# Performance work log

Hardware: AMD Instinct MI355X
Metric: run time of the kernel (lower is better)

## Reference

```python
import jax, jax.numpy as jnp
import numpy as np

B, T, D = 16, 4096, 768
S_MAX = 128  # max sentence (segment) count per sample


def setup_inputs() -> dict:
    key = jax.random.key(0)
    ks = jax.random.split(key, 8)
    hidden = jax.random.normal(ks[0], (B, T, D), dtype=jnp.float32)
    # sorted per-token segment ids == cumulative torch.split span structure
    seg_ids = jnp.sort(jax.random.randint(ks[1], (B, T), 0, S_MAX, dtype=jnp.int32), axis=-1)
    s1, s2, s3 = 1.0 / np.sqrt(D), 1.0 / np.sqrt(384), 1.0 / np.sqrt(128)
    W1 = jax.random.normal(ks[2], (D, 384), dtype=jnp.float32) * s1
    b1 = jnp.zeros((384,), dtype=jnp.float32)
    W2 = jax.random.normal(ks[3], (384, 128), dtype=jnp.float32) * s2
    b2 = jnp.zeros((128,), dtype=jnp.float32)
    W3 = jax.random.normal(ks[4], (128, 2), dtype=jnp.float32) * s3
    b3 = jnp.zeros((2,), dtype=jnp.float32)
    return {"hidden": hidden, "seg_ids": seg_ids, "W1": W1, "b1": b1,
            "W2": W2, "b2": b2, "W3": W3, "b3": b3}


def reference(hidden, seg_ids, W1, b1, W2, b2, W3, b3):
    # split_tensor: per-sample segment-sum over token spans, padded to S_MAX.
    # Segments with no tokens come out zero, matching F.pad of the torch code.
    sent_em = jax.vmap(
        lambda h, s: jax.ops.segment_sum(h, s, num_segments=S_MAX)
    )(hidden, seg_ids)  # [B, S_MAX, D]
    # sent_pred MLP head
    x = jax.nn.relu(jnp.einsum('bsd,df->bsf', sent_em, W1) + b1)
    x = jax.nn.relu(jnp.einsum('bsf,fg->bsg', x, W2) + b2)
    pred = jnp.einsum('bsg,gc->bsc', x, W3) + b3  # [B, S_MAX, 2]
    return pred.reshape(B * S_MAX, -1)
```

## Files before the change

### kernel.cpp

```cpp
#include <hip/hip_runtime.h>

#define BATCH 16
#define TOK   4096
#define DIM   768
#define SMAX  128
#define BM    8

__device__ __forceinline__ int lower_bound_i(const int* __restrict__ a, int n, int v) {
    int lo = 0, hi = n;
    while (lo < hi) {
        int m = (lo + hi) >> 1;
        if (a[m] < v) lo = m + 1; else hi = m;
    }
    return lo;
}

__device__ __forceinline__ float f4get(const float4& v, int k) {
    switch (k) {
        case 0: return v.x;
        case 1: return v.y;
        case 2: return v.z;
        default: return v.w;
    }
}

__device__ __forceinline__ void f2acc(float2& a, const float2& v) {
    a.x += v.x; a.y += v.y;
}

__global__ __launch_bounds__(192)
void bounds_kernel(const int* __restrict__ seg, int* __restrict__ bounds) {
    const int b = blockIdx.x;
    const int s = threadIdx.x;
    if (s <= SMAX)
        bounds[b * (SMAX + 1) + s] = lower_bound_i(seg + b * TOK, TOK, s);
}

__global__ __launch_bounds__(1024)
void fused_kernel(const float* __restrict__ hidden,
                  const int* __restrict__ bounds,
                  const float* __restrict__ W1, const float* __restrict__ b1,
                  const float* __restrict__ W2, const float* __restrict__ b2,
                  const float* __restrict__ W3, const float* __restrict__ b3,
                  float* __restrict__ out) {
    __shared__ __align__(16) float A [BM * DIM];
    __shared__ __align__(16) float X1[BM * 384];
    __shared__ __align__(16) float X2[BM * 128];
    __shared__ __align__(16) float P [8 * BM * 384];

    const int tid  = threadIdx.x;
    const int row0 = blockIdx.x * BM;
    const int b    = row0 / SMAX;
    const int s0   = row0 % SMAX;

    {
        const int grp  = tid >> 7;
        const int lane = tid & 127;

        const int lo = bounds[b * (SMAX + 1) + s0 + grp];
        const int hi = bounds[b * (SMAX + 1) + s0 + grp + 1];

        const float2* __restrict__ hp =
            reinterpret_cast<const float2*>(hidden + (size_t)b * TOK * DIM) + lane * 3;

        float2 a0 = make_float2(0.f, 0.f);
        float2 a1 = make_float2(0.f, 0.f);
        float2 a2 = make_float2(0.f, 0.f);

        int t = lo;
        for (; t + 12 <= hi; t += 12) {
            float2 v0[12], v1[12], v2[12];
            #pragma unroll
            for (int u = 0; u < 12; ++u) {
                const float2* p = hp + (size_t)(t + u) * 384;
                v0[u] = p[0]; v1[u] = p[1]; v2[u] = p[2];
            }
            #pragma unroll
            for (int u = 0; u < 12; ++u) {
                f2acc(a0, v0[u]); f2acc(a1, v1[u]); f2acc(a2, v2[u]);
            }
        }
        for (; t + 4 <= hi; t += 4) {
            float2 v0[4], v1[4], v2[4];
            #pragma unroll
            for (int u = 0; u < 4; ++u) {
                const float2* p = hp + (size_t)(t + u) * 384;
                v0[u] = p[0]; v1[u] = p[1]; v2[u] = p[2];
            }
            #pragma unroll
            for (int u = 0; u < 4; ++u) {
                f2acc(a0, v0[u]); f2acc(a1, v1[u]); f2acc(a2, v2[u]);
            }
        }
        for (; t < hi; ++t) {
            const float2* p = hp + (size_t)t * 384;
            f2acc(a0, p[0]); f2acc(a1, p[1]); f2acc(a2, p[2]);
        }

        float2* dA = reinterpret_cast<float2*>(&A[grp * DIM + lane * 6]);
        dA[0] = a0; dA[1] = a1; dA[2] = a2;
    }
    __syncthreads();

    const int c1 = tid & 127;
    const int kg = tid >> 7;

    {
        float acc[BM][3];
        #pragma unroll
        for (int r = 0; r < BM; ++r)
            #pragma unroll
            for (int j = 0; j < 3; ++j) acc[r][j] = 0.f;

        const int k0 = kg * 96;
        for (int k = k0; k < k0 + 96; k += 4) {
            float4 a[BM];
            #pragma unroll
            for (int r = 0; r < BM; ++r)
                a[r] = *reinterpret_cast<const float4*>(&A[r * DIM + k]);
            #pragma unroll
            for (int kk = 0; kk < 4; ++kk) {
                const float w0 = W1[(size_t)(k + kk) * 384 + c1];
                const float w1 = W1[(size_t)(k + kk) * 384 + c1 + 128];
                const float w2 = W1[(size_t)(k + kk) * 384 + c1 + 256];
                #pragma unroll
                for (int r = 0; r < BM; ++r) {
                    const float av = f4get(a[r], kk);
                    acc[r][0] = fmaf(av, w0, acc[r][0]);
                    acc[r][1] = fmaf(av, w1, acc[r][1]);
                    acc[r][2] = fmaf(av, w2, acc[r][2]);
                }
            }
        }
        #pragma unroll
        for (int r = 0; r < BM; ++r)
            #pragma unroll
            for (int j = 0; j < 3; ++j)
                P[(kg * BM + r) * 384 + c1 + j * 128] = acc[r][j];
    }
    __syncthreads();

    for (int i = tid; i < BM * 384; i += 1024) {
        const int row = i / 384;
        const int col = i - row * 384;
        float s = b1[col];
        #pragma unroll
        for (int g = 0; g < 8; ++g)
            s += P[(g * BM + row) * 384 + col];
        X1[i] = s > 0.f ? s : 0.f;
    }
    __syncthreads();

    {
        float acc2[BM];
        #pragma unroll
        for (int r = 0; r < BM; ++r) acc2[r] = 0.f;

        const int k0 = kg * 48;
        for (int k = k0; k < k0 + 48; k += 4) {
            float4 x[BM];
            #pragma unroll
            for (int r = 0; r < BM; ++r)
                x[r] = *reinterpret_cast<const float4*>(&X1[r * 384 + k]);
            #pragma unroll
            for (int kk = 0; kk < 4; ++kk) {
                const float w = W2[(size_t)(k + kk) * 128 + c1];
                #pragma unroll
                for (int r = 0; r < BM; ++r)
                    acc2[r] = fmaf(f4get(x[r], kk), w, acc2[r]);
            }
        }
        #pragma unroll
        for (int r = 0; r < BM; ++r)
            P[(kg * BM + r) * 128 + c1] = acc2[r];
    }
    __syncthreads();

    {
        const int row = tid >> 7;
        const int col = c1;
        float s = b2[col];
        #pragma unroll
        for (int g = 0; g < 8; ++g)
            s += P[(g * BM + row) * 128 + col];
        X2[row * 128 + col] = s > 0.f ? s : 0.f;
    }
    __syncthreads();

    if (tid < BM * 2) {
        const int r = tid >> 1;
        const int c = tid & 1;
        float sacc = 0.f;
        #pragma unroll 8
        for (int k = 0; k < 128; ++k)
            sacc = fmaf(X2[r * 128 + k], W3[k * 2 + c], sacc);
        out[(row0 + r) * 2 + c] = sacc + b3[c];
    }
}

extern "C" void kernel_launch(void* const* d_in, const int* in_sizes, int n_in,
                              void* d_out, int out_size, void* d_ws, size_t ws_size,
                              hipStream_t stream) {
    const float* hidden = (const float*)d_in[0];
    const int*   seg    = (const int*)d_in[1];
    const float* W1     = (const float*)d_in[2];
    const float* b1     = (const float*)d_in[3];
    const float* W2     = (const float*)d_in[4];
    const float* b2     = (const float*)d_in[5];
    const float* W3     = (const float*)d_in[6];
    const float* b3     = (const float*)d_in[7];
    float* out  = (float*)d_out;
    int* bounds = (int*)d_ws;

    bounds_kernel<<<BATCH, 192, 0, stream>>>(seg, bounds);
    fused_kernel<<<(BATCH * SMAX) / BM, 1024, 0, stream>>>(
        hidden, bounds, W1, b1, W2, b2, W3, b3, out);
}
```

Measured before the change: 67.43 us.

## Halve rows per block and split each segment's token range across two thread groups

Reduces BM from 8 to 4 so the grid doubles to 512 blocks. Each segment's token span is now split at its midpoint between two 128-thread groups, and the two partial sums are added when the A tile is read in the first GEMM. The 12-token unrolled load loop is removed, and a launch-bounds occupancy hint is added. The aim is more parallelism and memory-level concurrency in the bandwidth-bound segment sum. The cost is that every block reloads W1 and W2 for only 4 rows, doubling weight traffic, and the 4-deep unroll keeps fewer loads in flight per thread.

```diff
diff --git a/kernel.cpp b/kernel.cpp
--- a/kernel.cpp
+++ b/kernel.cpp
@@ -4,7 +4,7 @@
 #define TOK   4096
 #define DIM   768
 #define SMAX  128
-#define BM    8
+#define BM    4
 
 __device__ __forceinline__ int lower_bound_i(const int* __restrict__ a, int n, int v) {
     int lo = 0, hi = n;
@@ -36,17 +36,17 @@
         bounds[b * (SMAX + 1) + s] = lower_bound_i(seg + b * TOK, TOK, s);
 }
 
-__global__ __launch_bounds__(1024)
+__global__ __launch_bounds__(1024, 8)
 void fused_kernel(const float* __restrict__ hidden,
                   const int* __restrict__ bounds,
                   const float* __restrict__ W1, const float* __restrict__ b1,
                   const float* __restrict__ W2, const float* __restrict__ b2,
                   const float* __restrict__ W3, const float* __restrict__ b3,
                   float* __restrict__ out) {
-    __shared__ __align__(16) float A [BM * DIM];
+    __shared__ __align__(16) float A2[2 * BM * DIM];
+    __shared__ __align__(16) float P [8 * BM * 384];
     __shared__ __align__(16) float X1[BM * 384];
     __shared__ __align__(16) float X2[BM * 128];
-    __shared__ __align__(16) float P [8 * BM * 384];
 
     const int tid  = threadIdx.x;
     const int row0 = blockIdx.x * BM;
@@ -56,9 +56,14 @@
     {
         const int grp  = tid >> 7;
         const int lane = tid & 127;
-
-        const int lo = bounds[b * (SMAX + 1) + s0 + grp];
-        const int hi = bounds[b * (SMAX + 1) + s0 + grp + 1];
+        const int sg   = grp >> 1;
+        const int ph   = grp & 1;
+
+        const int lo  = bounds[b * (SMAX + 1) + s0 + sg];
+        const int hi  = bounds[b * (SMAX + 1) + s0 + sg + 1];
+        const int mid = (lo + hi) >> 1;
+        const int t0  = ph ? mid : lo;
+        const int t1  = ph ? hi  : mid;
 
         const float2* __restrict__ hp =
             reinterpret_cast<const float2*>(hidden + (size_t)b * TOK * DIM) + lane * 3;
@@ -67,20 +72,8 @@
         float2 a1 = make_float2(0.f, 0.f);
         float2 a2 = make_float2(0.f, 0.f);
 
-        int t = lo;
-        for (; t + 12 <= hi; t += 12) {
-            float2 v0[12], v1[12], v2[12];
-            #pragma unroll
-            for (int u = 0; u < 12; ++u) {
-                const float2* p = hp + (size_t)(t + u) * 384;
-                v0[u] = p[0]; v1[u] = p[1]; v2[u] = p[2];
-            }
-            #pragma unroll
-            for (int u = 0; u < 12; ++u) {
-                f2acc(a0, v0[u]); f2acc(a1, v1[u]); f2acc(a2, v2[u]);
-            }
-        }
-        for (; t + 4 <= hi; t += 4) {
+        int t = t0;
+        for (; t + 4 <= t1; t += 4) {
             float2 v0[4], v1[4], v2[4];
             #pragma unroll
             for (int u = 0; u < 4; ++u) {
@@ -92,12 +85,12 @@
                 f2acc(a0, v0[u]); f2acc(a1, v1[u]); f2acc(a2, v2[u]);
             }
         }
-        for (; t < hi; ++t) {
+        for (; t < t1; ++t) {
             const float2* p = hp + (size_t)t * 384;
             f2acc(a0, p[0]); f2acc(a1, p[1]); f2acc(a2, p[2]);
         }
 
-        float2* dA = reinterpret_cast<float2*>(&A[grp * DIM + lane * 6]);
+        float2* dA = reinterpret_cast<float2*>(&A2[(ph * BM + sg) * DIM + lane * 6]);
         dA[0] = a0; dA[1] = a1; dA[2] = a2;
     }
     __syncthreads();
@@ -116,8 +109,11 @@
         for (int k = k0; k < k0 + 96; k += 4) {
             float4 a[BM];
             #pragma unroll
-            for (int r = 0; r < BM; ++r)
-                a[r] = *reinterpret_cast<const float4*>(&A[r * DIM + k]);
+            for (int r = 0; r < BM; ++r) {
+                const float4 u = *reinterpret_cast<const float4*>(&A2[r * DIM + k]);
+                const float4 v = *reinterpret_cast<const float4*>(&A2[(BM + r) * DIM + k]);
+                a[r] = make_float4(u.x + v.x, u.y + v.y, u.z + v.z, u.w + v.w);
+            }
             #pragma unroll
             for (int kk = 0; kk < 4; ++kk) {
                 const float w0 = W1[(size_t)(k + kk) * 384 + c1];
@@ -176,7 +172,7 @@
     }
     __syncthreads();
 
-    {
+    if (tid < BM * 128) {
         const int row = tid >> 7;
         const int col = c1;
         float s = b2[col];
```

New measurement: 73.53 us. 9.1% more time.

## Balance token segment-sum across thread groups by splitting block token range evenly

Applied to the files above, without the earlier changes.

Instead of each 128-thread group summing one segment's tokens, the block's whole token range for its 8 segments is split evenly across the 8 groups. Each group writes partial sums for the segments at its range boundaries into scratch shared memory, and a merge pass then adds those partials into the segment rows. This removes load imbalance when segment lengths vary. It costs an extra zeroing pass, a merge pass, extra barriers, and uses a smaller 4-token unroll instead of 12.

```diff
diff --git a/kernel.cpp b/kernel.cpp
--- a/kernel.cpp
+++ b/kernel.cpp
@@ -47,63 +47,92 @@
     __shared__ __align__(16) float X1[BM * 384];
     __shared__ __align__(16) float X2[BM * 128];
     __shared__ __align__(16) float P [8 * BM * 384];
+    __shared__ int sbounds[BM + 1];
+    __shared__ int fseg[8], lseg[8];
+
+    float* Apart = P;
 
     const int tid  = threadIdx.x;
     const int row0 = blockIdx.x * BM;
     const int b    = row0 / SMAX;
     const int s0   = row0 % SMAX;
-
-    {
-        const int grp  = tid >> 7;
-        const int lane = tid & 127;
-
-        const int lo = bounds[b * (SMAX + 1) + s0 + grp];
-        const int hi = bounds[b * (SMAX + 1) + s0 + grp + 1];
+    const int grp  = tid >> 7;
+    const int lane = tid & 127;
+
+    if (tid <= BM) sbounds[tid] = bounds[b * (SMAX + 1) + s0 + tid];
+    if (tid < 8) { fseg[tid] = -1; lseg[tid] = -1; }
+    for (int i = tid; i < BM * DIM; i += 1024) A[i] = 0.f;
+    __syncthreads();
+
+    {
+        const int L = sbounds[0], H = sbounds[BM];
+        const int total = H - L;
+        const int t0 = L + ((total * grp) >> 3);
+        const int t1 = L + ((total * (grp + 1)) >> 3);
 
         const float2* __restrict__ hp =
             reinterpret_cast<const float2*>(hidden + (size_t)b * TOK * DIM) + lane * 3;
 
-        float2 a0 = make_float2(0.f, 0.f);
-        float2 a1 = make_float2(0.f, 0.f);
-        float2 a2 = make_float2(0.f, 0.f);
-
-        int t = lo;
-        for (; t + 12 <= hi; t += 12) {
-            float2 v0[12], v1[12], v2[12];
-            #pragma unroll
-            for (int u = 0; u < 12; ++u) {
-                const float2* p = hp + (size_t)(t + u) * 384;
-                v0[u] = p[0]; v1[u] = p[1]; v2[u] = p[2];
+        if (t0 < t1) {
+            int curs = 0;
+            while (sbounds[curs + 1] <= t0) ++curs;
+            const int sfirst = curs;
+            int t = t0;
+            while (t < t1) {
+                while (sbounds[curs + 1] <= t) ++curs;
+                const int send = min(t1, sbounds[curs + 1]);
+
+                float2 r0 = make_float2(0.f, 0.f);
+                float2 r1 = make_float2(0.f, 0.f);
+                float2 r2 = make_float2(0.f, 0.f);
+                for (; t + 4 <= send; t += 4) {
+                    float2 v0[4], v1[4], v2[4];
+                    #pragma unroll
+                    for (int u = 0; u < 4; ++u) {
+                        const float2* p = hp + (size_t)(t + u) * (DIM / 2);
+                        v0[u] = p[0]; v1[u] = p[1]; v2[u] = p[2];
+                    }
+                    #pragma unroll
+                    for (int u = 0; u < 4; ++u) {
+                        f2acc(r0, v0[u]); f2acc(r1, v1[u]); f2acc(r2, v2[u]);
+                    }
+                }
+                for (; t < send; ++t) {
+                    const float2* p = hp + (size_t)t * (DIM / 2);
+                    f2acc(r0, p[0]); f2acc(r1, p[1]); f2acc(r2, p[2]);
+                }
+
+                float2* dst;
+                if (curs == sfirst) {
+                    dst = reinterpret_cast<float2*>(&Apart[(grp * 2 + 0) * DIM]) + lane * 3;
+                    if (lane == 0) fseg[grp] = curs;
+                } else if (sbounds[curs + 1] > t1) {
+                    dst = reinterpret_cast<float2*>(&Apart[(grp * 2 + 1) * DIM]) + lane * 3;
+                    if (lane == 0) lseg[grp] = curs;
+                } else {
+                    dst = reinterpret_cast<float2*>(&A[curs * DIM]) + lane * 3;
+                }
+                dst[0] = r0; dst[1] = r1; dst[2] = r2;
             }
-            #pragma unroll
-            for (int u = 0; u < 12; ++u) {
-                f2acc(a0, v0[u]); f2acc(a1, v1[u]); f2acc(a2, v2[u]);
-            }
-        }
-        for (; t + 4 <= hi; t += 4) {
-            float2 v0[4], v1[4], v2[4];
-            #pragma unroll
-            for (int u = 0; u < 4; ++u) {
-                const float2* p = hp + (size_t)(t + u) * 384;
-                v0[u] = p[0]; v1[u] = p[1]; v2[u] = p[2];
-            }
-            #pragma unroll
-            for (int u = 0; u < 4; ++u) {
-                f2acc(a0, v0[u]); f2acc(a1, v1[u]); f2acc(a2, v2[u]);
-            }
-        }
-        for (; t < hi; ++t) {
-            const float2* p = hp + (size_t)t * 384;
-            f2acc(a0, p[0]); f2acc(a1, p[1]); f2acc(a2, p[2]);
-        }
-
-        float2* dA = reinterpret_cast<float2*>(&A[grp * DIM + lane * 6]);
-        dA[0] = a0; dA[1] = a1; dA[2] = a2;
-    }
-    __syncthreads();
-
-    const int c1 = tid & 127;
-    const int kg = tid >> 7;
+        }
+    }
+    __syncthreads();
+
+    for (int i = tid; i < BM * DIM; i += 1024) {
+        const int r = i / DIM;
+        const int col = i - r * DIM;
+        float v = A[i];
+        #pragma unroll
+        for (int g = 0; g < 8; ++g) {
+            if (fseg[g] == r) v += Apart[(g * 2 + 0) * DIM + col];
+            if (lseg[g] == r) v += Apart[(g * 2 + 1) * DIM + col];
+        }
+        A[i] = v;
+    }
+    __syncthreads();
+
+    const int c1 = lane;
+    const int kg = grp;
 
     {
         float acc[BM][3];
@@ -177,7 +206,7 @@
     __syncthreads();
 
     {
-        const int row = tid >> 7;
+        const int row = grp;
         const int col = c1;
         float s = b2[col];
         #pragma unroll
```

After: 70.70 us. 1.05x slower.

## Compute first MLP layer with bf16 MFMA using pre-transposed bf16 W1

Applied to the files above, without the earlier changes.

Adds a prep kernel that transposes W1 and converts it to bf16. The fused kernel now packs the segment sums into bf16 in shared memory, padded to 16 rows with zeros, and computes layer 1 with mfma_f32_16x16x32_bf16 on 12 waves. This removes the scalar FMA loop and the 8-way partial-sum reduction for layer 1, along with its large shared buffer. In exchange it adds an extra kernel launch on every call, half the MFMA rows are wasted on padding, and both the activations and W1 lose precision to bf16.

```diff
diff --git a/kernel.cpp b/kernel.cpp
--- a/kernel.cpp
+++ b/kernel.cpp
@@ -5,6 +5,9 @@
 #define DIM   768
 #define SMAX  128
 #define BM    8
+
+typedef float f32x4 __attribute__((ext_vector_type(4)));
+typedef short s16x8 __attribute__((ext_vector_type(8)));
 
 __device__ __forceinline__ int lower_bound_i(const int* __restrict__ a, int n, int v) {
     int lo = 0, hi = n;
@@ -28,6 +31,25 @@
     a.x += v.x; a.y += v.y;
 }
 
+__device__ __forceinline__ unsigned short bf16_rne(float f) {
+    unsigned int u = __float_as_uint(f);
+    u += 0x7FFFu + ((u >> 16) & 1u);
+    return (unsigned short)(u >> 16);
+}
+
+__device__ __forceinline__ unsigned int bf16_pack2(float f0, float f1) {
+    unsigned int u0 = __float_as_uint(f0) + 0x8000u;
+    unsigned int u1 = __float_as_uint(f1) + 0x8000u;
+    return (u0 >> 16) | (u1 & 0xFFFF0000u);
+}
+
+__global__ __launch_bounds__(768)
+void prep_w1t_kernel(const float* __restrict__ W1, unsigned short* __restrict__ W1T) {
+    const int c = blockIdx.x;
+    const int k = threadIdx.x;
+    W1T[c * 768 + k] = bf16_rne(W1[(size_t)k * 384 + c]);
+}
+
 __global__ __launch_bounds__(192)
 void bounds_kernel(const int* __restrict__ seg, int* __restrict__ bounds) {
     const int b = blockIdx.x;
@@ -39,24 +61,26 @@
 __global__ __launch_bounds__(1024)
 void fused_kernel(const float* __restrict__ hidden,
                   const int* __restrict__ bounds,
-                  const float* __restrict__ W1, const float* __restrict__ b1,
+                  const unsigned short* __restrict__ W1T, const float* __restrict__ b1,
                   const float* __restrict__ W2, const float* __restrict__ b2,
                   const float* __restrict__ W3, const float* __restrict__ b3,
                   float* __restrict__ out) {
-    __shared__ __align__(16) float A [BM * DIM];
+    __shared__ __align__(16) unsigned int A_bf32[16 * 388];
     __shared__ __align__(16) float X1[BM * 384];
     __shared__ __align__(16) float X2[BM * 128];
-    __shared__ __align__(16) float P [8 * BM * 384];
+    __shared__ __align__(16) float P2[8 * BM * 128];
 
     const int tid  = threadIdx.x;
     const int row0 = blockIdx.x * BM;
     const int b    = row0 / SMAX;
     const int s0   = row0 % SMAX;
-
-    {
-        const int grp  = tid >> 7;
-        const int lane = tid & 127;
-
+    const int grp  = tid >> 7;
+    const int lane = tid & 127;
+
+    for (int i = tid; i < 8 * 388; i += 1024)
+        A_bf32[8 * 388 + i] = 0u;
+
+    {
         const int lo = bounds[b * (SMAX + 1) + s0 + grp];
         const int hi = bounds[b * (SMAX + 1) + s0 + grp + 1];
 
@@ -97,60 +121,57 @@
             f2acc(a0, p[0]); f2acc(a1, p[1]); f2acc(a2, p[2]);
         }
 
-        float2* dA = reinterpret_cast<float2*>(&A[grp * DIM + lane * 6]);
-        dA[0] = a0; dA[1] = a1; dA[2] = a2;
-    }
-    __syncthreads();
-
-    const int c1 = tid & 127;
-    const int kg = tid >> 7;
-
-    {
-        float acc[BM][3];
-        #pragma unroll
-        for (int r = 0; r < BM; ++r)
-            #pragma unroll
-            for (int j = 0; j < 3; ++j) acc[r][j] = 0.f;
-
-        const int k0 = kg * 96;
-        for (int k = k0; k < k0 + 96; k += 4) {
-            float4 a[BM];
-            #pragma unroll
-            for (int r = 0; r < BM; ++r)
-                a[r] = *reinterpret_cast<const float4*>(&A[r * DIM + k]);
-            #pragma unroll
-            for (int kk = 0; kk < 4; ++kk) {
-                const float w0 = W1[(size_t)(k + kk) * 384 + c1];
-                const float w1 = W1[(size_t)(k + kk) * 384 + c1 + 128];
-                const float w2 = W1[(size_t)(k + kk) * 384 + c1 + 256];
+        const int base = grp * 388 + lane * 3;
+        A_bf32[base + 0] = bf16_pack2(a0.x, a0.y);
+        A_bf32[base + 1] = bf16_pack2(a1.x, a1.y);
+        A_bf32[base + 2] = bf16_pack2(a2.x, a2.y);
+    }
+    __syncthreads();
+
+    {
+        const int wid  = tid >> 6;
+        const int l    = tid & 63;
+        const int lrow = l & 15;
+        const int lg   = l >> 4;
+
+        if (wid < 12) {
+            const int n0 = wid * 32;
+            const int n1 = n0 + 16;
+            f32x4 acc0 = {0.f, 0.f, 0.f, 0.f};
+            f32x4 acc1 = {0.f, 0.f, 0.f, 0.f};
+
+            const unsigned int* abase = &A_bf32[lrow * 388 + lg * 4];
+            const unsigned short* w0p = W1T + (size_t)(n0 + lrow) * 768 + lg * 8;
+            const unsigned short* w1p = W1T + (size_t)(n1 + lrow) * 768 + lg * 8;
+
+            for (int ks = 0; ks < 24; ++ks) {
+                s16x8 af = *reinterpret_cast<const s16x8*>(abase + ks * 16);
+                s16x8 bf0 = *reinterpret_cast<const s16x8*>(w0p + ks * 32);
+                s16x8 bf1 = *reinterpret_cast<const s16x8*>(w1p + ks * 32);
+                acc0 = __builtin_amdgcn_mfma_f32_16x16x32_bf16(af, bf0, acc0, 0, 0, 0);
+                acc1 = __builtin_amdgcn_mfma_f32_16x16x32_bf16(af, bf1, acc1, 0, 0, 0);
+            }
+
+            if (lg < 2) {
+                const int c0 = n0 + lrow;
+                const int c1c = n1 + lrow;
+                const float bb0 = b1[c0];
+                const float bb1 = b1[c1c];
                 #pragma unroll
-                for (int r = 0; r < BM; ++r) {
-                    const float av = f4get(a[r], kk);
-                    acc[r][0] = fmaf(av, w0, acc[r][0]);
-                    acc[r][1] = fmaf(av, w1, acc[r][1]);
-                    acc[r][2] = fmaf(av, w2, acc[r][2]);
+                for (int r4 = 0; r4 < 4; ++r4) {
+                    const int row = lg * 4 + r4;
+                    const float v0 = acc0[r4] + bb0;
+                    const float v1 = acc1[r4] + bb1;
+                    X1[row * 384 + c0]  = v0 > 0.f ? v0 : 0.f;
+                    X1[row * 384 + c1c] = v1 > 0.f ? v1 : 0.f;
                 }
             }
         }
-        #pragma unroll
-        for (int r = 0; r < BM; ++r)
-            #pragma unroll
-            for (int j = 0; j < 3; ++j)
-                P[(kg * BM + r) * 384 + c1 + j * 128] = acc[r][j];
-    }
-    __syncthreads();
-
-    for (int i = tid; i < BM * 384; i += 1024) {
-        const int row = i / 384;
-        const int col = i - row * 384;
-        float s = b1[col];
-        #pragma unroll
-        for (int g = 0; g < 8; ++g)
-            s += P[(g * BM + row) * 384 + col];
-        X1[i] = s > 0.f ? s : 0.f;
-    }
-    __syncthreads();
-
+    }
+    __syncthreads();
+
+    const int c1 = lane;
+    const int kg = grp;
     {
         float acc2[BM];
         #pragma unroll
@@ -172,17 +193,17 @@
         }
         #pragma unroll
         for (int r = 0; r < BM; ++r)
-            P[(kg * BM + r) * 128 + c1] = acc2[r];
-    }
-    __syncthreads();
-
-    {
-        const int row = tid >> 7;
+            P2[(kg * BM + r) * 128 + c1] = acc2[r];
+    }
+    __syncthreads();
+
+    {
+        const int row = grp;
         const int col = c1;
         float s = b2[col];
         #pragma unroll
         for (int g = 0; g < 8; ++g)
-            s += P[(g * BM + row) * 128 + col];
+            s += P2[(g * BM + row) * 128 + col];
         X2[row * 128 + col] = s > 0.f ? s : 0.f;
     }
     __syncthreads();
@@ -209,10 +230,13 @@
     const float* b2     = (const float*)d_in[5];
     const float* W3     = (const float*)d_in[6];
     const float* b3     = (const float*)d_in[7];
-    float* out  = (float*)d_out;
+    float* out = (float*)d_out;
+
     int* bounds = (int*)d_ws;
-
+    unsigned short* W1T = (unsigned short*)((char*)d_ws + 16384);
+
+    prep_w1t_kernel<<<384, 768, 0, stream>>>(W1, W1T);
     bounds_kernel<<<BATCH, 192, 0, stream>>>(seg, bounds);
     fused_kernel<<<(BATCH * SMAX) / BM, 1024, 0, stream>>>(
-        hidden, bounds, W1, b1, W2, b2, W3, b3, out);
-}
+        hidden, bounds, W1T, b1, W2, b2, W3, b3, out);
+}
```

Measured after the change: 66.02 us. 2.1% less time.
